# Kernel tuning notes

Hardware: AMD Instinct MI355X
Metric: run time of the kernel (lower is better)

Reference implementation:

```python
import jax, jax.numpy as jnp
import numpy as np

N = 50000       # nodes
E = 600000      # directed edges (before self loops)
IN_CH = 128
HID = 64
HEADS = 2
H2_CH = HID // HEADS  # 32
OUT_CH = 96
NEG_SLOPE = 0.2


def _w(key, shape):
    fan_in = shape[-1]
    return jax.random.normal(key, shape, dtype=jnp.float32) / np.sqrt(fan_in).astype(np.float32)


def setup_inputs() -> dict:
    key = jax.random.key(0)
    ks = jax.random.split(key, 20)
    x = jax.random.normal(ks[0], (N, IN_CH), dtype=jnp.float32)
    edge_index = jax.random.randint(ks[1], (2, E), 0, N, dtype=jnp.int32)
    batch = jnp.zeros((N,), dtype=jnp.int32)
    return {
        "x": x, "edge_index": edge_index, "batch": batch,
        # lin_in 128->128
        "Win": _w(ks[2], (IN_CH, IN_CH)), "b_in": jnp.zeros((IN_CH,), jnp.float32),
        # conv1: GATv2Conv(128 -> 64, heads=2, concat=True)
        "Wl1": _w(ks[3], (HEADS * HID, IN_CH)), "bl1": jnp.zeros((HEADS * HID,), jnp.float32),
        "Wr1": _w(ks[4], (HEADS * HID, IN_CH)), "br1": jnp.zeros((HEADS * HID,), jnp.float32),
        "att1": _w(ks[5], (HEADS, HID)), "bias1": jnp.zeros((HEADS * HID,), jnp.float32),
        # conv2: GATv2Conv(128 -> 32, heads=1, concat=True)
        "Wl2": _w(ks[6], (H2_CH, HEADS * HID)), "bl2": jnp.zeros((H2_CH,), jnp.float32),
        "Wr2": _w(ks[7], (H2_CH, HEADS * HID)), "br2": jnp.zeros((H2_CH,), jnp.float32),
        "att2": _w(ks[8], (1, H2_CH)), "bias2": jnp.zeros((H2_CH,), jnp.float32),
        # final linear 32 -> 96
        "Wout": _w(ks[9], (OUT_CH, H2_CH)), "b_out": jnp.zeros((OUT_CH,), jnp.float32),
    }


def _segment_softmax(logits, seg, num):
    # logits: [E, H] grouped by seg (destination node); every node has a self loop.
    m = jax.ops.segment_max(logits, seg, num_segments=num)
    ex = jnp.exp(logits - m[seg])
    s = jax.ops.segment_sum(ex, seg, num_segments=num)
    return ex / s[seg]


def _gatv2_conv(h, Wl, bl, Wr, br, att, bias, src, dst, heads, ch):
    n = h.shape[0]
    xl = (h @ Wl.T + bl).reshape(n, heads, ch)  # source-side (x_j)
    xr = (h @ Wr.T + br).reshape(n, heads, ch)  # target-side (x_i)
    e = jax.nn.leaky_relu(xl[src] + xr[dst], NEG_SLOPE)       # [E, H, C]
    logits = jnp.einsum('ehc,hc->eh', e, att)                  # [E, H]
    alpha = _segment_softmax(logits, dst, n)                   # softmax over in-edges per dst
    out = jax.ops.segment_sum(alpha[:, :, None] * xl[src], dst, num_segments=n)
    return out.reshape(n, heads * ch) + bias


def reference(x, edge_index, batch, Win, b_in, Wl1, bl1, Wr1, br1, att1, bias1,
              Wl2, bl2, Wr2, br2, att2, bias2, Wout, b_out):
    n = x.shape[0]
    loops = jnp.arange(n, dtype=edge_index.dtype)
    src = jnp.concatenate([edge_index[0], loops])  # add_self_loops=True (PyG default)
    dst = jnp.concatenate([edge_index[1], loops])
    h = x @ Win.T + b_in
    h = jax.nn.relu(_gatv2_conv(h, Wl1, bl1, Wr1, br1, att1, bias1, src, dst, HEADS, HID))
    h = jax.nn.relu(_gatv2_conv(h, Wl2, bl2, Wr2, br2, att2, bias2, src, dst, 1, H2_CH))
    num_graphs = 1
    sums = jax.ops.segment_sum(h, batch, num_segments=num_graphs)          # [G, 32]
    cnt = jax.ops.segment_sum(jnp.ones((n,), h.dtype), batch, num_segments=num_graphs)
    pooled = sums / cnt[:, None]
    return pooled @ Wout.T + b_out  # [G, 96]
```

## Files before the change

### kernel.cpp

```cpp
#include <hip/hip_runtime.h>
#include <hip/hip_bf16.h>
#include <math.h>


#define NEG_SLOPE 0.2f
#define LOG2E 1.4426950408889634f
#define NREP 16
#define ELLW 64
#define CH 2048
#define CAPB 8192

typedef __attribute__((ext_vector_type(8))) short bf16x8;
typedef __attribute__((ext_vector_type(4))) float f32x4;

__device__ __forceinline__ float leaky(float t) { return fmaxf(t, NEG_SLOPE * t); }
__device__ __forceinline__ float bf2f(unsigned short u) {
    return __uint_as_float((unsigned)u << 16);
}
__device__ __forceinline__ short f2bf(float f) {
    __hip_bfloat16 h = __float2bfloat16(f);
    return *reinterpret_cast<short*>(&h);
}
__device__ __forceinline__ short f2bf_fast(float f) {
    return (short)((__float_as_uint(f) + 0x8000u) >> 16);
}

__global__ __launch_bounds__(256) void prep_kernel(const float* __restrict__ Win,
                                                   const float* __restrict__ b_in,
                                                   const float* __restrict__ Wl1,
                                                   const float* __restrict__ bl1,
                                                   const float* __restrict__ Wr1,
                                                   const float* __restrict__ br1,
                                                   const float* __restrict__ Wl2,
                                                   const float* __restrict__ bl2,
                                                   const float* __restrict__ Wr2,
                                                   const float* __restrict__ br2,
                                                   unsigned short* __restrict__ Wcat1,
                                                   float* __restrict__ bcat1,
                                                   unsigned short* __restrict__ Wcat2,
                                                   float* __restrict__ bcat2,
                                                   int* __restrict__ bucketCnt,
                                                   float* __restrict__ pooledR, int N) {
    int b = blockIdx.x, t = threadIdx.x;
    if (b < 128) {
        int half = t >> 7;
        int k = t & 127;
        int o = b * 2 + half;
        const float* Wx = (o < 128) ? Wl1 : Wr1;
        const float* bx = (o < 128) ? bl1 : br1;
        int oo = o & 127;
        float acc = 0.f;
#pragma unroll 16
        for (int j = 0; j < 128; ++j)
            acc = fmaf(Wx[oo * 128 + j], Win[j * 128 + k], acc);
        Wcat1[o * 128 + k] = (unsigned short)f2bf(acc);

        __shared__ float red[256];
        red[t] = Wx[oo * 128 + k] * b_in[k];
        __syncthreads();
        for (int off = 64; off > 0; off >>= 1) {
            if (k < off) red[t] += red[t + off];
            __syncthreads();
        }
        if (k == 0) bcat1[o] = red[half * 128] + bx[oo];
    } else if (b < 160) {
        int i = (b - 128) * 256 + t;
        int m = i >> 7, kk = i & 127;
        float v = (m < 32) ? Wl2[m * 128 + kk] : Wr2[(m - 32) * 128 + kk];
        Wcat2[i] = (unsigned short)f2bf(v);
        if (b == 128 && t < 64) bcat2[t] = (t < 32) ? bl2[t] : br2[t - 32];
    } else if (b == 160) {
        if (t < 256) bucketCnt[t] = 0;
    } else {
        int i = (b - 161) * 256 + t;
        if (i < NREP * 32) pooledR[i] = 0.f;
    }
}

__global__ __launch_bounds__(256) void part_kernel(const int* __restrict__ ei,
                                                   int* __restrict__ bucketCnt,
                                                   unsigned int* __restrict__ region,
                                                   int E) {
    __shared__ int hist[256];
    __shared__ int base[256];
    __shared__ int off[256];
    int b = blockIdx.x, t = threadIdx.x;
    int e0 = b * CH;
    int e1 = e0 + CH; if (e1 > E) e1 = E;

    hist[t] = 0;
    __syncthreads();
    for (int e = e0 + t; e < e1; e += 256) {
        int d = ei[E + e];
        atomicAdd(&hist[d >> 8], 1);
    }
    __syncthreads();
    int h = hist[t];
    base[t] = (h > 0) ? atomicAdd(&bucketCnt[t], h) : 0;
    off[t] = 0;
    __syncthreads();
    for (int e = e0 + t; e < e1; e += 256) {
        int s = ei[e];
        int d = ei[E + e];
        int bk = d >> 8;
        int p = base[bk] + atomicAdd(&off[bk], 1);
        if (p < CAPB)
            region[(size_t)bk * CAPB + p] = (unsigned)s | ((unsigned)(d & 255) << 16);
    }
}

__global__ __launch_bounds__(256) void ellb_kernel(const unsigned int* __restrict__ region,
                                                   const int* __restrict__ bucketCnt,
                                                   unsigned short* __restrict__ ell,
                                                   int* __restrict__ deg, int N) {
    __shared__ unsigned short tile[256 * ELLW];
    __shared__ int cur[256];
    int nb = blockIdx.x, t = threadIdx.x;
    cur[t] = 0;
    __syncthreads();
    int cnt = bucketCnt[nb];
    if (cnt > CAPB) cnt = CAPB;
    for (int i = t; i < cnt; i += 256) {
        unsigned p = region[(size_t)nb * CAPB + i];
        int doff = p >> 16;
        int s = p & 0xFFFF;
        int r = atomicAdd(&cur[doff], 1);
        if (r < ELLW) tile[doff * ELLW + r] = (unsigned short)s;
    }
    __syncthreads();
    int node = nb * 256 + t;
    int dgl = cur[t];
    if (dgl > ELLW) dgl = ELLW;
    if (node < N) {
        deg[node] = dgl;
        int pe = dgl + 8; if (pe > ELLW) pe = ELLW;
        for (int r = dgl; r < pe; ++r) tile[t * ELLW + r] = (unsigned short)node;
    }
    __syncthreads();
    const uint4* tl = (const uint4*)tile;
    uint4* gl = (uint4*)(ell + (size_t)nb * 256 * ELLW);
#pragma unroll
    for (int k = 0; k < 8; ++k) {
        int idx = t + k * 256;
        int row = idx >> 3;
        if (nb * 256 + row < N) gl[idx] = tl[idx];
    }
}

__global__ __launch_bounds__(256) void gemm1_kernel(const float* __restrict__ x,
                                                    const unsigned short* __restrict__ W,
                                                    const float* __restrict__ bias,
                                                    unsigned short* __restrict__ XL,
                                                    unsigned short* __restrict__ XR, int N) {
    const int w = threadIdx.x >> 6;
    const int lane = threadIdx.x & 63;
    const int ln = lane & 15;
    const int quad = lane >> 4;
    const int nb = blockIdx.x * 32;
    const int c0 = w * 64;

    int rows[2];
#pragma unroll
    for (int rt = 0; rt < 2; ++rt) {
        int n = nb + rt * 16 + ln;
        rows[rt] = n < N ? n : N - 1;
    }

    float4 araw[2][4][2];
#pragma unroll
    for (int rt = 0; rt < 2; ++rt)
#pragma unroll
        for (int kc = 0; kc < 4; ++kc) {
            const float* p = x + (size_t)rows[rt] * 128 + kc * 32 + quad * 8;
            araw[rt][kc][0] = *(const float4*)p;
            araw[rt][kc][1] = *(const float4*)(p + 4);
        }
    bf16x8 a[2][4];
#pragma unroll
    for (int rt = 0; rt < 2; ++rt)
#pragma unroll
        for (int kc = 0; kc < 4; ++kc) {
            float4 u = araw[rt][kc][0], v = araw[rt][kc][1];
            a[rt][kc][0] = f2bf_fast(u.x); a[rt][kc][1] = f2bf_fast(u.y);
            a[rt][kc][2] = f2bf_fast(u.z); a[rt][kc][3] = f2bf_fast(u.w);
            a[rt][kc][4] = f2bf_fast(v.x); a[rt][kc][5] = f2bf_fast(v.y);
            a[rt][kc][6] = f2bf_fast(v.z); a[rt][kc][7] = f2bf_fast(v.w);
        }

    f32x4 acc[2][4];
#pragma unroll
    for (int rt = 0; rt < 2; ++rt)
#pragma unroll
        for (int ct = 0; ct < 4; ++ct) acc[rt][ct] = (f32x4){0.f, 0.f, 0.f, 0.f};

#pragma unroll
    for (int kc = 0; kc < 4; ++kc) {
        const int k0 = kc * 32 + quad * 8;
        bf16x8 wv[4];
#pragma unroll
        for (int ct = 0; ct < 4; ++ct)
            wv[ct] = *(const bf16x8*)(W + (size_t)(c0 + ct * 16 + ln) * 128 + k0);
#pragma unroll
        for (int rt = 0; rt < 2; ++rt)
#pragma unroll
            for (int ct = 0; ct < 4; ++ct)
                acc[rt][ct] = __builtin_amdgcn_mfma_f32_16x16x32_bf16(wv[ct], a[rt][kc], acc[rt][ct], 0, 0, 0);
    }

#pragma unroll
    for (int rt = 0; rt < 2; ++rt) {
        int n = nb + rt * 16 + ln;
        if (n >= N) continue;
#pragma unroll
        for (int ct = 0; ct < 4; ++ct) {
            int cb = c0 + ct * 16 + quad * 4;
            float4 bv = *(const float4*)&bias[cb];
            ushort4 o;
            o.x = (unsigned short)f2bf(acc[rt][ct][0] + bv.x);
            o.y = (unsigned short)f2bf(acc[rt][ct][1] + bv.y);
            o.z = (unsigned short)f2bf(acc[rt][ct][2] + bv.z);
            o.w = (unsigned short)f2bf(acc[rt][ct][3] + bv.w);
            if (cb < 128) *(ushort4*)&XL[(size_t)n * 128 + cb] = o;
            else          *(ushort4*)&XR[(size_t)n * 128 + cb - 128] = o;
        }
    }
}

__global__ __launch_bounds__(256) void gemm2_kernel(const unsigned short* __restrict__ A,
                                                    const unsigned short* __restrict__ W,
                                                    const float* __restrict__ bias,
                                                    unsigned short* __restrict__ OUT0,
                                                    unsigned short* __restrict__ OUT1,
                                                    int N) {
    const int w = threadIdx.x >> 6;
    const int lane = threadIdx.x & 63;
    const int ln = lane & 15;
    const int quad = lane >> 4;
    const int nb = blockIdx.x * 64;
    const int c0 = w * 16;

    f32x4 acc[4];
#pragma unroll
    for (int rt = 0; rt < 4; ++rt) acc[rt] = (f32x4){0.f, 0.f, 0.f, 0.f};

    int rows[4];
#pragma unroll
    for (int rt = 0; rt < 4; ++rt) {
        int n = nb + rt * 16 + ln;
        rows[rt] = n < N ? n : N - 1;
    }

#pragma unroll
    for (int kc = 0; kc < 4; ++kc) {
        const int k0 = kc * 32 + quad * 8;
        bf16x8 a[4];
#pragma unroll
        for (int rt = 0; rt < 4; ++rt)
            a[rt] = *(const bf16x8*)(A + (size_t)rows[rt] * 128 + k0);
        bf16x8 wv = *(const bf16x8*)(W + (size_t)(c0 + ln) * 128 + k0);
#pragma unroll
        for (int rt = 0; rt < 4; ++rt)
            acc[rt] = __builtin_amdgcn_mfma_f32_16x16x32_bf16(wv, a[rt], acc[rt], 0, 0, 0);
    }

#pragma unroll
    for (int rt = 0; rt < 4; ++rt) {
        int n = nb + rt * 16 + ln;
        if (n >= N) continue;
        int cb = c0 + quad * 4;
        float4 bv = *(const float4*)&bias[cb];
        ushort4 o;
        o.x = (unsigned short)f2bf(acc[rt][0] + bv.x);
        o.y = (unsigned short)f2bf(acc[rt][1] + bv.y);
        o.z = (unsigned short)f2bf(acc[rt][2] + bv.z);
        o.w = (unsigned short)f2bf(acc[rt][3] + bv.w);
        if (cb < 32) *(ushort4*)&OUT0[(size_t)n * 32 + cb] = o;
        else         *(ushort4*)&OUT1[(size_t)n * 32 + cb - 32] = o;
    }
}

__global__ __launch_bounds__(256) void node_conv1(const unsigned short* __restrict__ XL,
                                                  const unsigned short* __restrict__ XR,
                                                  const int* __restrict__ deg,
                                                  const unsigned short* __restrict__ ell,
                                                  const float* __restrict__ att,
                                                  const float* __restrict__ bias,
                                                  unsigned short* __restrict__ H1, int N) {
    int d = blockIdx.x * 8 + (threadIdx.x >> 5);
    if (d >= N) return;
    int l = threadIdx.x & 31;
    int c0 = 4 * l;
    const unsigned short* row = ell + (size_t)d * ELLW;
    int re = deg[d];

    float4 attv = *(const float4*)&att[c0];
    attv.x *= LOG2E; attv.y *= LOG2E; attv.z *= LOG2E; attv.w *= LOG2E;
    ushort4 xru = *(const ushort4*)&XR[(size_t)d * 128 + c0];
    float xr0 = bf2f(xru.x), xr1 = bf2f(xru.y), xr2 = bf2f(xru.z), xr3 = bf2f(xru.w);

    float ssum = 0.f, a0 = 0.f, a1 = 0.f, a2 = 0.f, a3 = 0.f;

#define LOADX1(j) (*(const ushort4*)&XL[(size_t)row[j] * 128 + c0])
#define PROC1(xu)                                                          \
    {                                                                      \
        float x0 = bf2f(xu.x), x1 = bf2f(xu.y), x2 = bf2f(xu.z), x3 = bf2f(xu.w); \
        float p = leaky(x0 + xr0) * attv.x;                                \
        p = fmaf(leaky(x1 + xr1), attv.y, p);                              \
        p = fmaf(leaky(x2 + xr2), attv.z, p);                              \
        p = fmaf(leaky(x3 + xr3), attv.w, p);                              \
        p += __shfl_xor(p, 8, 16);                                         \
        p += __shfl_xor(p, 4, 16);                                         \
        p += __shfl_xor(p, 2, 16);                                         \
        p += __shfl_xor(p, 1, 16);                                         \
        float wgt = exp2f(p);                                              \
        ssum += wgt;                                                       \
        a0 = fmaf(wgt, x0, a0); a1 = fmaf(wgt, x1, a1);                    \
        a2 = fmaf(wgt, x2, a2); a3 = fmaf(wgt, x3, a3);                    \
    }

    {
        ushort4 xls = *(const ushort4*)&XL[(size_t)d * 128 + c0];
        PROC1(xls);
    }
    if (re > 0) {
        ushort4 b0 = LOADX1(0), b1 = LOADX1(1), b2 = LOADX1(2), b3 = LOADX1(3);
        for (int j = 0; j < re; j += 4) {
            int j4 = j + 4 < ELLW - 3 ? j + 4 : ELLW - 4;
            ushort4 n0 = LOADX1(j4), n1 = LOADX1(j4 + 1), n2 = LOADX1(j4 + 2), n3 = LOADX1(j4 + 3);
            PROC1(b0);
            if (j + 1 < re) PROC1(b1);
            if (j + 2 < re) PROC1(b2);
            if (j + 3 < re) PROC1(b3);
            b0 = n0; b1 = n1; b2 = n2; b3 = n3;
        }
    }
#undef PROC1
#undef LOADX1

    float inv = 1.0f / ssum;
    float4 bv = *(const float4*)&bias[c0];
    float r0 = fmaf(a0, inv, bv.x), r1 = fmaf(a1, inv, bv.y);
    float r2 = fmaf(a2, inv, bv.z), r3 = fmaf(a3, inv, bv.w);
    ushort4 o;
    o.x = (unsigned short)f2bf(r0 > 0.f ? r0 : 0.f);
    o.y = (unsigned short)f2bf(r1 > 0.f ? r1 : 0.f);
    o.z = (unsigned short)f2bf(r2 > 0.f ? r2 : 0.f);
    o.w = (unsigned short)f2bf(r3 > 0.f ? r3 : 0.f);
    *(ushort4*)&H1[(size_t)d * 128 + c0] = o;
}

__global__ __launch_bounds__(256) void node_conv2(const unsigned short* __restrict__ XL,
                                                  const unsigned short* __restrict__ XR,
                                                  const int* __restrict__ deg,
                                                  const unsigned short* __restrict__ ell,
                                                  const float* __restrict__ att,
                                                  const float* __restrict__ bias,
                                                  float* __restrict__ pooledR, int N) {
    __shared__ float psh[32];
    if (threadIdx.x < 32) psh[threadIdx.x] = 0.0f;
    __syncthreads();

    int slot = threadIdx.x >> 3;
    int l = threadIdx.x & 7;
    int c0 = 4 * l;
    float4 attv = *(const float4*)&att[c0];
    attv.x *= LOG2E; attv.y *= LOG2E; attv.z *= LOG2E; attv.w *= LOG2E;
    float4 bv = *(const float4*)&bias[c0];
    float p0 = 0.f, p1 = 0.f, p2 = 0.f, p3 = 0.f;

#define LOADX2(j) (*(const ushort4*)&XL[(size_t)row[j] * 32 + c0])
#define PROC2(xu)                                                          \
    {                                                                      \
        float x0 = bf2f(xu.x), x1 = bf2f(xu.y), x2 = bf2f(xu.z), x3 = bf2f(xu.w); \
        float p = leaky(x0 + xr0) * attv.x;                                \
        p = fmaf(leaky(x1 + xr1), attv.y, p);                              \
        p = fmaf(leaky(x2 + xr2), attv.z, p);                              \
        p = fmaf(leaky(x3 + xr3), attv.w, p);                              \
        p += __shfl_xor(p, 4, 8);                                          \
        p += __shfl_xor(p, 2, 8);                                          \
        p += __shfl_xor(p, 1, 8);                                          \
        float wgt = exp2f(p);                                              \
        ssum += wgt;                                                       \
        a0 = fmaf(wgt, x0, a0); a1 = fmaf(wgt, x1, a1);                    \
        a2 = fmaf(wgt, x2, a2); a3 = fmaf(wgt, x3, a3);                    \
    }

    for (int d = blockIdx.x * 32 + slot; d < N; d += gridDim.x * 32) {
        const unsigned short* row = ell + (size_t)d * ELLW;
        int re = deg[d];
        ushort4 xru = *(const ushort4*)&XR[(size_t)d * 32 + c0];
        float xr0 = bf2f(xru.x), xr1 = bf2f(xru.y), xr2 = bf2f(xru.z), xr3 = bf2f(xru.w);
        float ssum = 0.f, a0 = 0.f, a1 = 0.f, a2 = 0.f, a3 = 0.f;

        {
            ushort4 xls = *(const ushort4*)&XL[(size_t)d * 32 + c0];
            PROC2(xls);
        }
        if (re > 0) {
            ushort4 b0 = LOADX2(0), b1 = LOADX2(1), b2 = LOADX2(2), b3 = LOADX2(3);
            for (int j = 0; j < re; j += 4) {
                int j4 = j + 4 < ELLW - 3 ? j + 4 : ELLW - 4;
                ushort4 n0 = LOADX2(j4), n1 = LOADX2(j4 + 1), n2 = LOADX2(j4 + 2), n3 = LOADX2(j4 + 3);
                PROC2(b0);
                if (j + 1 < re) PROC2(b1);
                if (j + 2 < re) PROC2(b2);
                if (j + 3 < re) PROC2(b3);
                b0 = n0; b1 = n1; b2 = n2; b3 = n3;
            }
        }

        float inv = 1.0f / ssum;
        float r0 = fmaf(a0, inv, bv.x), r1 = fmaf(a1, inv, bv.y);
        float r2 = fmaf(a2, inv, bv.z), r3 = fmaf(a3, inv, bv.w);
        p0 += r0 > 0.f ? r0 : 0.f;
        p1 += r1 > 0.f ? r1 : 0.f;
        p2 += r2 > 0.f ? r2 : 0.f;
        p3 += r3 > 0.f ? r3 : 0.f;
    }
#undef PROC2
#undef LOADX2
    atomicAdd(&psh[c0 + 0], p0);
    atomicAdd(&psh[c0 + 1], p1);
    atomicAdd(&psh[c0 + 2], p2);
    atomicAdd(&psh[c0 + 3], p3);
    __syncthreads();
    float* rep = pooledR + (blockIdx.x & (NREP - 1)) * 32;
    if (threadIdx.x < 32) atomicAdd(&rep[threadIdx.x], psh[threadIdx.x]);
}

__global__ void out_kernel(const float* __restrict__ pooledR, const float* __restrict__ Wout,
                           const float* __restrict__ b_out, float* __restrict__ out, int N) {
    __shared__ float psum[32];
    if (threadIdx.x < 32) {
        float tot = 0.f;
#pragma unroll
        for (int r = 0; r < NREP; ++r) tot += pooledR[r * 32 + threadIdx.x];
        psum[threadIdx.x] = tot;
    }
    __syncthreads();
    int m = threadIdx.x;
    if (m < 96) {
        float invN = 1.0f / (float)N;
        float s = b_out[m];
#pragma unroll
        for (int c = 0; c < 32; ++c) s += (psum[c] * invN) * Wout[m * 32 + c];
        out[m] = s;
    }
}

extern "C" void kernel_launch(void* const* d_in, const int* in_sizes, int n_in,
                              void* d_out, int out_size, void* d_ws, size_t ws_size,
                              hipStream_t stream) {
    const float* x     = (const float*)d_in[0];
    const int*   ei    = (const int*)d_in[1];
    const float* Win   = (const float*)d_in[3];
    const float* b_in  = (const float*)d_in[4];
    const float* Wl1   = (const float*)d_in[5];
    const float* bl1   = (const float*)d_in[6];
    const float* Wr1   = (const float*)d_in[7];
    const float* br1   = (const float*)d_in[8];
    const float* att1  = (const float*)d_in[9];
    const float* bias1 = (const float*)d_in[10];
    const float* Wl2   = (const float*)d_in[11];
    const float* bl2   = (const float*)d_in[12];
    const float* Wr2   = (const float*)d_in[13];
    const float* br2   = (const float*)d_in[14];
    const float* att2  = (const float*)d_in[15];
    const float* bias2 = (const float*)d_in[16];
    const float* Wout  = (const float*)d_in[17];
    const float* b_out = (const float*)d_in[18];
    float* out = (float*)d_out;

    int N = in_sizes[0] / 128;
    int E = in_sizes[1] / 2;
    int NB = (N + 255) >> 8;

    char* wsb = (char*)d_ws;
    size_t off = 0;
    auto alloc = [&](size_t bytes) { void* p = wsb + off; off += (bytes + 255) & ~(size_t)255; return p; };

    unsigned short* XL1   = (unsigned short*)alloc((size_t)N * 128 * 2);
    unsigned short* XR1   = (unsigned short*)alloc((size_t)N * 128 * 2);
    unsigned short* H1    = (unsigned short*)alloc((size_t)N * 128 * 2);
    unsigned short* Wcat1 = (unsigned short*)alloc(256 * 128 * 2);
    unsigned short* Wcat2 = (unsigned short*)alloc(64 * 128 * 2);
    float* bcat1   = (float*)alloc(256 * 4);
    float* bcat2   = (float*)alloc(64 * 4);
    float* pooledR = (float*)alloc(NREP * 32 * 4);
    int* bucketCnt = (int*)alloc(256 * 4);
    int* deg       = (int*)alloc((size_t)N * 4);
    unsigned int* region = (unsigned int*)alloc((size_t)NB * CAPB * 4);
    unsigned short* ell  = (unsigned short*)alloc((size_t)N * ELLW * 2);
    unsigned short* XL2 = XL1;
    unsigned short* XR2 = XR1;

    prep_kernel<<<163, 256, 0, stream>>>(Win, b_in, Wl1, bl1, Wr1, br1,
                                         Wl2, bl2, Wr2, br2,
                                         Wcat1, bcat1, Wcat2, bcat2, bucketCnt, pooledR, N);
    part_kernel<<<(E + CH - 1) / CH, 256, 0, stream>>>(ei, bucketCnt, region, E);
    ellb_kernel<<<NB, 256, 0, stream>>>(region, bucketCnt, ell, deg, N);
    gemm1_kernel<<<(N + 31) / 32, 256, 0, stream>>>(x, Wcat1, bcat1, XL1, XR1, N);
    node_conv1<<<(N + 7) / 8, 256, 0, stream>>>(XL1, XR1, deg, ell, att1, bias1, H1, N);
    gemm2_kernel<<<(N + 63) / 64, 256, 0, stream>>>(H1, Wcat2, bcat2, XL2, XR2, N);
    node_conv2<<<1024, 256, 0, stream>>>(XL2, XR2, deg, ell, att2, bias2, pooledR, N);
    out_kernel<<<1, 128, 0, stream>>>(pooledR, Wout, b_out, out, N);
}
```

Baseline: 224.5 us.

## Fuse conv2 projection GEMM into node_conv1 epilogue via shared memory

Each node_conv1 block now writes its 8 aggregated H1 rows to shared memory and immediately multiplies them by Wcat2 with MFMA, producing XL2/XR2 directly. This removes the separate gemm2 launch and the global write/read of the N×128 bf16 H1 buffer. In exchange, each block wastes half of every 16-row MFMA tile (only 8 real rows), reloads the weight matrix per block, and adds a block-wide barrier that stalls warps with short neighbor lists. XL2/XR2 become separate buffers instead of aliasing XL1/XR1.

```diff
diff --git a/kernel.cpp b/kernel.cpp
--- a/kernel.cpp
+++ b/kernel.cpp
@@ -226,79 +226,32 @@
     }
 }
 
-__global__ __launch_bounds__(256) void gemm2_kernel(const unsigned short* __restrict__ A,
-                                                    const unsigned short* __restrict__ W,
-                                                    const float* __restrict__ bias,
-                                                    unsigned short* __restrict__ OUT0,
-                                                    unsigned short* __restrict__ OUT1,
-                                                    int N) {
-    const int w = threadIdx.x >> 6;
-    const int lane = threadIdx.x & 63;
-    const int ln = lane & 15;
-    const int quad = lane >> 4;
-    const int nb = blockIdx.x * 64;
-    const int c0 = w * 16;
-
-    f32x4 acc[4];
-#pragma unroll
-    for (int rt = 0; rt < 4; ++rt) acc[rt] = (f32x4){0.f, 0.f, 0.f, 0.f};
-
-    int rows[4];
-#pragma unroll
-    for (int rt = 0; rt < 4; ++rt) {
-        int n = nb + rt * 16 + ln;
-        rows[rt] = n < N ? n : N - 1;
-    }
-
-#pragma unroll
-    for (int kc = 0; kc < 4; ++kc) {
-        const int k0 = kc * 32 + quad * 8;
-        bf16x8 a[4];
-#pragma unroll
-        for (int rt = 0; rt < 4; ++rt)
-            a[rt] = *(const bf16x8*)(A + (size_t)rows[rt] * 128 + k0);
-        bf16x8 wv = *(const bf16x8*)(W + (size_t)(c0 + ln) * 128 + k0);
-#pragma unroll
-        for (int rt = 0; rt < 4; ++rt)
-            acc[rt] = __builtin_amdgcn_mfma_f32_16x16x32_bf16(wv, a[rt], acc[rt], 0, 0, 0);
-    }
-
-#pragma unroll
-    for (int rt = 0; rt < 4; ++rt) {
-        int n = nb + rt * 16 + ln;
-        if (n >= N) continue;
-        int cb = c0 + quad * 4;
-        float4 bv = *(const float4*)&bias[cb];
-        ushort4 o;
-        o.x = (unsigned short)f2bf(acc[rt][0] + bv.x);
-        o.y = (unsigned short)f2bf(acc[rt][1] + bv.y);
-        o.z = (unsigned short)f2bf(acc[rt][2] + bv.z);
-        o.w = (unsigned short)f2bf(acc[rt][3] + bv.w);
-        if (cb < 32) *(ushort4*)&OUT0[(size_t)n * 32 + cb] = o;
-        else         *(ushort4*)&OUT1[(size_t)n * 32 + cb - 32] = o;
-    }
-}
-
 __global__ __launch_bounds__(256) void node_conv1(const unsigned short* __restrict__ XL,
                                                   const unsigned short* __restrict__ XR,
                                                   const int* __restrict__ deg,
                                                   const unsigned short* __restrict__ ell,
                                                   const float* __restrict__ att,
                                                   const float* __restrict__ bias,
-                                                  unsigned short* __restrict__ H1, int N) {
-    int d = blockIdx.x * 8 + (threadIdx.x >> 5);
-    if (d >= N) return;
+                                                  const unsigned short* __restrict__ Wcat2,
+                                                  const float* __restrict__ bcat2,
+                                                  unsigned short* __restrict__ XL2,
+                                                  unsigned short* __restrict__ XR2, int N) {
+    __shared__ unsigned short hsh[8 * 128];
+    int g = threadIdx.x >> 5;
+    int d = blockIdx.x * 8 + g;
     int l = threadIdx.x & 31;
     int c0 = 4 * l;
-    const unsigned short* row = ell + (size_t)d * ELLW;
-    int re = deg[d];
-
-    float4 attv = *(const float4*)&att[c0];
-    attv.x *= LOG2E; attv.y *= LOG2E; attv.z *= LOG2E; attv.w *= LOG2E;
-    ushort4 xru = *(const ushort4*)&XR[(size_t)d * 128 + c0];
-    float xr0 = bf2f(xru.x), xr1 = bf2f(xru.y), xr2 = bf2f(xru.z), xr3 = bf2f(xru.w);
-
-    float ssum = 0.f, a0 = 0.f, a1 = 0.f, a2 = 0.f, a3 = 0.f;
+
+    if (d < N) {
+        const unsigned short* row = ell + (size_t)d * ELLW;
+        int re = deg[d];
+
+        float4 attv = *(const float4*)&att[c0];
+        attv.x *= LOG2E; attv.y *= LOG2E; attv.z *= LOG2E; attv.w *= LOG2E;
+        ushort4 xru = *(const ushort4*)&XR[(size_t)d * 128 + c0];
+        float xr0 = bf2f(xru.x), xr1 = bf2f(xru.y), xr2 = bf2f(xru.z), xr3 = bf2f(xru.w);
+
+        float ssum = 0.f, a0 = 0.f, a1 = 0.f, a2 = 0.f, a3 = 0.f;
 
 #define LOADX1(j) (*(const ushort4*)&XL[(size_t)row[j] * 128 + c0])
 #define PROC1(xu)                                                          \
@@ -318,35 +271,68 @@
         a2 = fmaf(wgt, x2, a2); a3 = fmaf(wgt, x3, a3);                    \
     }
 
-    {
-        ushort4 xls = *(const ushort4*)&XL[(size_t)d * 128 + c0];
-        PROC1(xls);
-    }
-    if (re > 0) {
-        ushort4 b0 = LOADX1(0), b1 = LOADX1(1), b2 = LOADX1(2), b3 = LOADX1(3);
-        for (int j = 0; j < re; j += 4) {
-            int j4 = j + 4 < ELLW - 3 ? j + 4 : ELLW - 4;
-            ushort4 n0 = LOADX1(j4), n1 = LOADX1(j4 + 1), n2 = LOADX1(j4 + 2), n3 = LOADX1(j4 + 3);
-            PROC1(b0);
-            if (j + 1 < re) PROC1(b1);
-            if (j + 2 < re) PROC1(b2);
-            if (j + 3 < re) PROC1(b3);
-            b0 = n0; b1 = n1; b2 = n2; b3 = n3;
-        }
-    }
+        {
+            ushort4 xls = *(const ushort4*)&XL[(size_t)d * 128 + c0];
+            PROC1(xls);
+        }
+        if (re > 0) {
+            ushort4 b0 = LOADX1(0), b1 = LOADX1(1), b2 = LOADX1(2), b3 = LOADX1(3);
+            for (int j = 0; j < re; j += 4) {
+                int j4 = j + 4 < ELLW - 3 ? j + 4 : ELLW - 4;
+                ushort4 n0 = LOADX1(j4), n1 = LOADX1(j4 + 1), n2 = LOADX1(j4 + 2), n3 = LOADX1(j4 + 3);
+                PROC1(b0);
+                if (j + 1 < re) PROC1(b1);
+                if (j + 2 < re) PROC1(b2);
+                if (j + 3 < re) PROC1(b3);
+                b0 = n0; b1 = n1; b2 = n2; b3 = n3;
+            }
+        }
 #undef PROC1
 #undef LOADX1
 
-    float inv = 1.0f / ssum;
-    float4 bv = *(const float4*)&bias[c0];
-    float r0 = fmaf(a0, inv, bv.x), r1 = fmaf(a1, inv, bv.y);
-    float r2 = fmaf(a2, inv, bv.z), r3 = fmaf(a3, inv, bv.w);
-    ushort4 o;
-    o.x = (unsigned short)f2bf(r0 > 0.f ? r0 : 0.f);
-    o.y = (unsigned short)f2bf(r1 > 0.f ? r1 : 0.f);
-    o.z = (unsigned short)f2bf(r2 > 0.f ? r2 : 0.f);
-    o.w = (unsigned short)f2bf(r3 > 0.f ? r3 : 0.f);
-    *(ushort4*)&H1[(size_t)d * 128 + c0] = o;
+        float inv = 1.0f / ssum;
+        float4 bv = *(const float4*)&bias[c0];
+        float r0 = fmaf(a0, inv, bv.x), r1 = fmaf(a1, inv, bv.y);
+        float r2 = fmaf(a2, inv, bv.z), r3 = fmaf(a3, inv, bv.w);
+        ushort4 o;
+        o.x = (unsigned short)f2bf(r0 > 0.f ? r0 : 0.f);
+        o.y = (unsigned short)f2bf(r1 > 0.f ? r1 : 0.f);
+        o.z = (unsigned short)f2bf(r2 > 0.f ? r2 : 0.f);
+        o.w = (unsigned short)f2bf(r3 > 0.f ? r3 : 0.f);
+        *(ushort4*)&hsh[g * 128 + c0] = o;
+    } else {
+        *(ushort4*)&hsh[g * 128 + c0] = make_ushort4(0, 0, 0, 0);
+    }
+    __syncthreads();
+
+    {
+        int w = threadIdx.x >> 6;
+        int lane = threadIdx.x & 63;
+        int ln = lane & 15;
+        int quad = lane >> 4;
+        f32x4 acc = (f32x4){0.f, 0.f, 0.f, 0.f};
+#pragma unroll
+        for (int kc = 0; kc < 4; ++kc) {
+            int k0 = kc * 32 + quad * 8;
+            bf16x8 a;
+            if (ln < 8) a = *(const bf16x8*)&hsh[ln * 128 + k0];
+            else        a = (bf16x8){0, 0, 0, 0, 0, 0, 0, 0};
+            bf16x8 wv = *(const bf16x8*)(Wcat2 + (size_t)(w * 16 + ln) * 128 + k0);
+            acc = __builtin_amdgcn_mfma_f32_16x16x32_bf16(wv, a, acc, 0, 0, 0);
+        }
+        int n = blockIdx.x * 8 + ln;
+        if (ln < 8 && n < N) {
+            int cb = w * 16 + quad * 4;
+            float4 bv = *(const float4*)&bcat2[cb];
+            ushort4 o;
+            o.x = (unsigned short)f2bf(acc[0] + bv.x);
+            o.y = (unsigned short)f2bf(acc[1] + bv.y);
+            o.z = (unsigned short)f2bf(acc[2] + bv.z);
+            o.w = (unsigned short)f2bf(acc[3] + bv.w);
+            if (cb < 32) *(ushort4*)&XL2[(size_t)n * 32 + cb] = o;
+            else         *(ushort4*)&XR2[(size_t)n * 32 + cb - 32] = o;
+        }
+    }
 }
 
 __global__ __launch_bounds__(256) void node_conv2(const unsigned short* __restrict__ XL,
@@ -481,7 +467,8 @@
 
     unsigned short* XL1   = (unsigned short*)alloc((size_t)N * 128 * 2);
     unsigned short* XR1   = (unsigned short*)alloc((size_t)N * 128 * 2);
-    unsigned short* H1    = (unsigned short*)alloc((size_t)N * 128 * 2);
+    unsigned short* XL2   = (unsigned short*)alloc((size_t)N * 32 * 2);
+    unsigned short* XR2   = (unsigned short*)alloc((size_t)N * 32 * 2);
     unsigned short* Wcat1 = (unsigned short*)alloc(256 * 128 * 2);
     unsigned short* Wcat2 = (unsigned short*)alloc(64 * 128 * 2);
     float* bcat1   = (float*)alloc(256 * 4);
@@ -491,8 +478,6 @@
     int* deg       = (int*)alloc((size_t)N * 4);
     unsigned int* region = (unsigned int*)alloc((size_t)NB * CAPB * 4);
     unsigned short* ell  = (unsigned short*)alloc((size_t)N * ELLW * 2);
-    unsigned short* XL2 = XL1;
-    unsigned short* XR2 = XR1;
 
     prep_kernel<<<163, 256, 0, stream>>>(Win, b_in, Wl1, bl1, Wr1, br1,
                                          Wl2, bl2, Wr2, br2,
@@ -500,8 +485,8 @@
     part_kernel<<<(E + CH - 1) / CH, 256, 0, stream>>>(ei, bucketCnt, region, E);
     ellb_kernel<<<NB, 256, 0, stream>>>(region, bucketCnt, ell, deg, N);
     gemm1_kernel<<<(N + 31) / 32, 256, 0, stream>>>(x, Wcat1, bcat1, XL1, XR1, N);
-    node_conv1<<<(N + 7) / 8, 256, 0, stream>>>(XL1, XR1, deg, ell, att1, bias1, H1, N);
-    gemm2_kernel<<<(N + 63) / 64, 256, 0, stream>>>(H1, Wcat2, bcat2, XL2, XR2, N);
+    node_conv1<<<(N + 7) / 8, 256, 0, stream>>>(XL1, XR1, deg, ell, att1, bias1,
+                                                Wcat2, bcat2, XL2, XR2, N);
     node_conv2<<<1024, 256, 0, stream>>>(XL2, XR2, deg, ell, att2, bias2, pooledR, N);
     out_kernel<<<1, 128, 0, stream>>>(pooledR, Wout, b_out, out, N);
 }
```

Result: faster. 220.0 us (-2.0%).
